# Optimization experiments

Measured on AMD Instinct MI355X. Metric: run time of the kernel, lower is better.

Reference implementation:

```python
import jax, jax.numpy as jnp
import numpy as np

NUM_SAMPLES = 128  # from __init__ default


def _trilinear_sample(vox, g):
    """grid_sample 5D, mode=bilinear (trilinear), padding_mode=zeros, align_corners=True.
    vox: [C, Dv, Hv, Wv]; g: [P, 3] normalized (x,y,z) with x->Wv, y->Hv, z->Dv.
    Returns [P, C]."""
    C, D, Hh, Ww = vox.shape
    x = (g[:, 0] + 1.0) * 0.5 * (Ww - 1)
    y = (g[:, 1] + 1.0) * 0.5 * (Hh - 1)
    z = (g[:, 2] + 1.0) * 0.5 * (D - 1)
    x0 = jnp.floor(x); y0 = jnp.floor(y); z0 = jnp.floor(z)
    xd = x - x0; yd = y - y0; zd = z - z0
    x0i = x0.astype(jnp.int32); y0i = y0.astype(jnp.int32); z0i = z0.astype(jnp.int32)
    out = jnp.zeros((g.shape[0], C), vox.dtype)
    for dz, wz in ((0, 1.0 - zd), (1, zd)):
        for dy, wy in ((0, 1.0 - yd), (1, yd)):
            for dx, wx in ((0, 1.0 - xd), (1, xd)):
                zi = z0i + dz; yi = y0i + dy; xi = x0i + dx
                valid = ((zi >= 0) & (zi < D) & (yi >= 0) & (yi < Hh) & (xi >= 0) & (xi < Ww)).astype(vox.dtype)
                zc = jnp.clip(zi, 0, D - 1); yc = jnp.clip(yi, 0, Hh - 1); xc = jnp.clip(xi, 0, Ww - 1)
                vals = vox[:, zc, yc, xc]  # [C, P]
                out = out + ((wz * wy * wx * valid)[:, None]) * vals.T
    return out


def setup_inputs() -> dict:
    key = jax.random.key(0)
    k1, k2 = jax.random.split(key)
    B, Hv, Wv, Dv = 4, 128, 128, 128
    H, W = 128, 128
    rgbsigma = jax.random.uniform(k1, (B, Hv, Wv, Dv, 4), dtype=jnp.float32)
    # cameras at ~z=3 looking down -z (identity rotation), slightly jittered
    pose = jnp.tile(jnp.eye(4, dtype=jnp.float32), (B, 1, 1))
    trans = jnp.array([0.0, 0.0, 3.0], dtype=jnp.float32) + 0.1 * jax.random.normal(k2, (B, 3), dtype=jnp.float32)
    pose = pose.at[:, :3, 3].set(trans)
    K = jnp.tile(jnp.array([[150.0, 0.0, 64.0], [0.0, 150.0, 64.0], [0.0, 0.0, 1.0]], dtype=jnp.float32), (B, 1, 1))
    bbox_min = jnp.tile(jnp.array([-1.0, -1.0, -1.0], dtype=jnp.float32), (B, 1))
    bbox_max = jnp.tile(jnp.array([1.0, 1.0, 1.0], dtype=jnp.float32), (B, 1))
    return {"rgbsigma": rgbsigma, "camera_pose": pose, "camera_intrinsics": K,
            "bbox_min": bbox_min, "bbox_max": bbox_max, "H": H, "W": W}


def reference(rgbsigma, camera_pose, camera_intrinsics, bbox_min, bbox_max, H, W):
    B = camera_pose.shape[0]
    N = H * W
    # --- ray generation ---
    ii, jj = jnp.meshgrid(jnp.arange(H, dtype=jnp.float32), jnp.arange(W, dtype=jnp.float32), indexing='ij')
    ii = ii.reshape(-1); jj = jj.reshape(-1)  # [N]
    fx = camera_intrinsics[:, 0, 0][:, None]; fy = camera_intrinsics[:, 1, 1][:, None]
    cx = camera_intrinsics[:, 0, 2][:, None]; cy = camera_intrinsics[:, 1, 2][:, None]
    dirs = jnp.stack([(jj[None, :] - cx) / fx, -(ii[None, :] - cy) / fy,
                      -jnp.ones((B, N), dtype=jnp.float32)], axis=-1)  # [B,N,3]
    rays_d = jnp.einsum('bij,bnj->bni', camera_pose[:, :3, :3], dirs)
    rays_d = rays_d / jnp.maximum(jnp.linalg.norm(rays_d, axis=-1, keepdims=True), 1e-12)
    rays_o = jnp.broadcast_to(camera_pose[:, None, :3, 3], (B, N, 3))
    # --- near/far via slab test ---
    inv_d = 1.0 / (rays_d + 1e-10)
    bmin = bbox_min[:, None, :]; bmax = bbox_max[:, None, :]
    t_min = (bmin - rays_o) * inv_d; t_max = (bmax - rays_o) * inv_d
    t1 = jnp.minimum(t_min, t_max); t2 = jnp.maximum(t_min, t_max)
    near = jnp.maximum(jnp.max(t1, axis=-1, keepdims=True), 0.1)
    far = jnp.maximum(jnp.min(t2, axis=-1, keepdims=True), near + 0.1)
    # --- stratified-uniform sample points ---
    t_vals = jnp.linspace(0.0, 1.0, NUM_SAMPLES, dtype=jnp.float32)
    z_vals = near + (far - near) * t_vals  # [B,N,M]
    pts = rays_o[:, :, None, :] + rays_d[:, :, None, :] * z_vals[..., None]  # [B,N,M,3]
    # --- trilinear voxel query ---
    scale = (bbox_max - bbox_min + 1e-10)[:, None, None, :]
    pts_norm = 2.0 * (pts - bbox_min[:, None, None, :]) / scale - 1.0
    vox = jnp.transpose(rgbsigma, (0, 4, 3, 1, 2))  # [B,4,Dv,Hv,Wv]
    sampled = jax.vmap(_trilinear_sample)(vox, pts_norm.reshape(B, N * NUM_SAMPLES, 3))
    sampled = sampled.reshape(B, N, NUM_SAMPLES, 4)
    rgb = sampled[..., :3]; sigma = sampled[..., 3]
    # --- alpha compositing ---
    dists = z_vals[..., 1:] - z_vals[..., :-1]
    dists = jnp.concatenate([dists, jnp.full_like(dists[..., :1], 1e10)], axis=-1)
    alpha = 1.0 - jnp.exp(-jax.nn.relu(sigma) * dists)
    trans = jnp.cumprod(jnp.concatenate([jnp.ones_like(alpha[..., :1]), 1.0 - alpha + 1e-10], axis=-1), axis=-1)[..., :-1]
    weights = alpha * trans
    rgb_map = jnp.sum(weights[..., None] * rgb, axis=-2)  # [B,N,3]
    acc_map = jnp.sum(weights, axis=-1)
    rgb_map = rgb_map + (1.0 - acc_map[..., None])  # white background
    return jnp.transpose(rgb_map.reshape(B, H, W, 3), (0, 3, 1, 2))
```

## Files before the change

### kernel.cpp

```cpp
#include <hip/hip_runtime.h>

#define NSAMP 128
#define VD 128
#define WPB 4

struct Corner8 {
    float4 v0, v1, v2, v3, v4, v5, v6, v7;
    float  w0, w1, w2, w3, w4, w5, w6, w7;
};

__device__ __forceinline__ void compute_ray_setup(
    int ray, int N, int W,
    const float* __restrict__ pose, const float* __restrict__ Kmat,
    const float* __restrict__ bmin, const float* __restrict__ bmax,
    float& axv, float& bxv, float& ayv, float& byv, float& azv, float& bzv,
    float& near, float& dt)
{
    const int b = ray / N;
    const int pix = ray - b * N;
    const int i = pix / W;
    const int j = pix - i * W;

    const float* P  = pose + b * 16;
    const float* Kb = Kmat + b * 9;
    const float fx = Kb[0], cx = Kb[2], fy = Kb[4], cy = Kb[5];

    const float dcx = ((float)j - cx) / fx;
    const float dcy = -((float)i - cy) / fy;
    const float dcz = -1.0f;

    float dx = P[0]*dcx + P[1]*dcy + P[2]*dcz;
    float dy = P[4]*dcx + P[5]*dcy + P[6]*dcz;
    float dz = P[8]*dcx + P[9]*dcy + P[10]*dcz;
    float nrm = sqrtf(dx*dx + dy*dy + dz*dz);
    nrm = fmaxf(nrm, 1e-12f);
    dx /= nrm; dy /= nrm; dz /= nrm;

    const float ox = P[3], oy = P[7], oz = P[11];

    const float bx0 = bmin[b*3+0], by0 = bmin[b*3+1], bz0 = bmin[b*3+2];
    const float bx1 = bmax[b*3+0], by1 = bmax[b*3+1], bz1 = bmax[b*3+2];

    const float ivx = 1.0f / (dx + 1e-10f);
    const float ivy = 1.0f / (dy + 1e-10f);
    const float ivz = 1.0f / (dz + 1e-10f);

    float ta, tb;
    ta = (bx0 - ox) * ivx; tb = (bx1 - ox) * ivx;
    const float t1x = fminf(ta, tb), t2x = fmaxf(ta, tb);
    ta = (by0 - oy) * ivy; tb = (by1 - oy) * ivy;
    const float t1y = fminf(ta, tb), t2y = fmaxf(ta, tb);
    ta = (bz0 - oz) * ivz; tb = (bz1 - oz) * ivz;
    const float t1z = fminf(ta, tb), t2z = fmaxf(ta, tb);

    near = fmaxf(fmaxf(t1x, fmaxf(t1y, t1z)), 0.1f);
    const float far = fmaxf(fminf(t2x, fminf(t2y, t2z)), near + 0.1f);

    const float sxs = (bx1 - bx0) + 1e-10f;
    const float sys = (by1 - by0) + 1e-10f;
    const float szs = (bz1 - bz0) + 1e-10f;
    const float C = (float)(VD - 1);
    axv = (ox - bx0) / sxs * C; bxv = dx / sxs * C;
    ayv = (oy - by0) / sys * C; byv = dy / sys * C;
    azv = (oz - bz0) / szs * C; bzv = dz / szs * C;

    dt = (far - near) * (1.0f / (float)(NSAMP - 1));
}

__global__ __launch_bounds__(256)
void RaySetup_kernel(const float* __restrict__ pose,
                     const float* __restrict__ Kmat,
                     const float* __restrict__ bmin,
                     const float* __restrict__ bmax,
                     const int* __restrict__ dH,
                     const int* __restrict__ dW,
                     float* __restrict__ rp,
                     int rays)
{
    const int ray = blockIdx.x * blockDim.x + threadIdx.x;
    if (ray >= rays) return;
    const int H = dH[0], W = dW[0];
    const int N = H * W;
    float axv, bxv, ayv, byv, azv, bzv, near, dt;
    compute_ray_setup(ray, N, W, pose, Kmat, bmin, bmax,
                      axv, bxv, ayv, byv, azv, bzv, near, dt);
    float4* o = reinterpret_cast<float4*>(rp + (size_t)ray * 8);
    o[0] = make_float4(axv, bxv, ayv, byv);
    o[1] = make_float4(azv, bzv, near, dt);
}

__device__ __forceinline__ void fetch_sample(
    Corner8& Bf, const float4* __restrict__ V4, float t,
    float axv, float bxv, float ayv, float byv, float azv, float bzv)
{
    const float xf = axv + bxv * t;
    const float yf = ayv + byv * t;
    const float zf = azv + bzv * t;
    const float x0f = floorf(xf), y0f = floorf(yf), z0f = floorf(zf);
    const float xd = xf - x0f, yd = yf - y0f, zd = zf - z0f;
    const int x0 = (int)x0f, y0 = (int)y0f, z0 = (int)z0f;
    const int x1 = x0 + 1, y1 = y0 + 1, z1 = z0 + 1;

    const int xc0 = min(max(x0, 0), VD - 1), xc1 = min(max(x1, 0), VD - 1);
    const int yc0 = min(max(y0, 0), VD - 1), yc1 = min(max(y1, 0), VD - 1);
    const int zc0 = min(max(z0, 0), VD - 1), zc1 = min(max(z1, 0), VD - 1);

    const float vx0 = (x0 == xc0) ? 1.0f : 0.0f;
    const float vx1 = (x1 == xc1) ? 1.0f : 0.0f;
    const float vy0 = (y0 == yc0) ? 1.0f : 0.0f;
    const float vy1 = (y1 == yc1) ? 1.0f : 0.0f;
    const float vz0 = (z0 == zc0) ? 1.0f : 0.0f;
    const float vz1 = (z1 == zc1) ? 1.0f : 0.0f;

    const float wx0 = (1.0f - xd) * vx0, wx1 = xd * vx1;
    const float wy0 = (1.0f - yd) * vy0, wy1 = yd * vy1;
    const float wz0 = (1.0f - zd) * vz0, wz1 = zd * vz1;

    const int r0 = yc0 << 14, r1 = yc1 << 14;
    const int c0 = xc0 << 7,  c1 = xc1 << 7;
    const int i00 = r0 + c0, i01 = r0 + c1;
    const int i10 = r1 + c0, i11 = r1 + c1;

    Bf.v0 = V4[i00 + zc0];
    Bf.v1 = V4[i00 + zc1];
    Bf.v2 = V4[i01 + zc0];
    Bf.v3 = V4[i01 + zc1];
    Bf.v4 = V4[i10 + zc0];
    Bf.v5 = V4[i10 + zc1];
    Bf.v6 = V4[i11 + zc0];
    Bf.v7 = V4[i11 + zc1];

    Bf.w0 = wy0 * wx0 * wz0;
    Bf.w1 = wy0 * wx0 * wz1;
    Bf.w2 = wy0 * wx1 * wz0;
    Bf.w3 = wy0 * wx1 * wz1;
    Bf.w4 = wy1 * wx0 * wz0;
    Bf.w5 = wy1 * wx0 * wz1;
    Bf.w6 = wy1 * wx1 * wz0;
    Bf.w7 = wy1 * wx1 * wz1;
}

__device__ __forceinline__ float4 interp_sample(const Corner8& Bf)
{
    float4 r;
    r.x = (Bf.w0*Bf.v0.x + Bf.w1*Bf.v1.x) + (Bf.w2*Bf.v2.x + Bf.w3*Bf.v3.x)
        + (Bf.w4*Bf.v4.x + Bf.w5*Bf.v5.x) + (Bf.w6*Bf.v6.x + Bf.w7*Bf.v7.x);
    r.y = (Bf.w0*Bf.v0.y + Bf.w1*Bf.v1.y) + (Bf.w2*Bf.v2.y + Bf.w3*Bf.v3.y)
        + (Bf.w4*Bf.v4.y + Bf.w5*Bf.v5.y) + (Bf.w6*Bf.v6.y + Bf.w7*Bf.v7.y);
    r.z = (Bf.w0*Bf.v0.z + Bf.w1*Bf.v1.z) + (Bf.w2*Bf.v2.z + Bf.w3*Bf.v3.z)
        + (Bf.w4*Bf.v4.z + Bf.w5*Bf.v5.z) + (Bf.w6*Bf.v6.z + Bf.w7*Bf.v7.z);
    r.w = (Bf.w0*Bf.v0.w + Bf.w1*Bf.v1.w) + (Bf.w2*Bf.v2.w + Bf.w3*Bf.v3.w)
        + (Bf.w4*Bf.v4.w + Bf.w5*Bf.v5.w) + (Bf.w6*Bf.v6.w + Bf.w7*Bf.v7.w);
    return r;
}

__device__ __forceinline__ float scan_prod64(float v, int lane)
{
    #pragma unroll
    for (int d = 1; d < 64; d <<= 1) {
        const float o = __shfl_up(v, d, 64);
        if (lane >= d) v *= o;
    }
    return v;
}

template <bool USE_WS>
__global__ __launch_bounds__(256, 1)
void VoxelRenderer_kernel(const float* __restrict__ vol,
                          const float* __restrict__ pose,
                          const float* __restrict__ Kmat,
                          const float* __restrict__ bmin,
                          const float* __restrict__ bmax,
                          const int* __restrict__ dH,
                          const int* __restrict__ dW,
                          const float* __restrict__ rayp,
                          float* __restrict__ out,
                          int rays)
{
    const int lane = threadIdx.x & 63;
    const int wid  = threadIdx.x >> 6;

    const int nwg = gridDim.x;
    const int bid = blockIdx.x;
    const int q = nwg >> 3, r = nwg & 7;
    const int xcd = bid & 7, idx = bid >> 3;
    const int swz = (xcd < r ? xcd * (q + 1) : r * (q + 1) + (xcd - r) * q) + idx;

    const int ray = swz * WPB + wid;
    if (ray >= rays) return;

    const int H = dH[0], W = dW[0];
    const int N = H * W;
    const int b = ray / N;
    const int pix = ray - b * N;

    float axv, bxv, ayv, byv, azv, bzv, near, dt;
    if (USE_WS) {
        const float4* p = reinterpret_cast<const float4*>(rayp + (size_t)ray * 8);
        const float4 p0 = p[0];
        const float4 p1 = p[1];
        axv = p0.x; bxv = p0.y; ayv = p0.z; byv = p0.w;
        azv = p1.x; bzv = p1.y; near = p1.z; dt = p1.w;
    } else {
        compute_ray_setup(ray, N, W, pose, Kmat, bmin, bmax,
                          axv, bxv, ayv, byv, azv, bzv, near, dt);
    }

    const float4* __restrict__ V4 =
        reinterpret_cast<const float4*>(vol + (size_t)b * VD * VD * VD * 4);

    const float tA = near + dt * (float)lane;
    const float tB = tA + dt * 64.0f;

    Corner8 A, Bf;
    fetch_sample(A,  V4, tA, axv, bxv, ayv, byv, azv, bzv);
    fetch_sample(Bf, V4, tB, axv, bxv, ayv, byv, azv, bzv);

    const float4 sA = interp_sample(A);
    const float sigA = fmaxf(sA.w, 0.0f);
    const float alphaA = 1.0f - __expf(-sigA * dt);
    const float tmA = 1.0f - alphaA + 1e-10f;

    float inclA = scan_prod64(tmA, lane);
    float PA = __shfl_up(inclA, 1, 64);
    if (lane == 0) PA = 1.0f;
    const float TtotA = __shfl(inclA, 63, 64);

    const float4 sB = interp_sample(Bf);
    const float sigB = fmaxf(sB.w, 0.0f);
    const float distB = (lane == 63) ? 1e10f : dt;
    const float alphaB = 1.0f - __expf(-sigB * distB);
    const float tmB = 1.0f - alphaB + 1e-10f;

    float inclB = scan_prod64(tmB, lane);
    float PB = __shfl_up(inclB, 1, 64);
    if (lane == 0) PB = 1.0f;
    const float TtotB = __shfl(inclB, 63, 64);

    const float wA = alphaA * PA;
    const float wB = alphaB * PB * TtotA;

    float R  = wA * sA.x + wB * sB.x;
    float G  = wA * sA.y + wB * sB.y;
    float Bl = wA * sA.z + wB * sB.z;

    #pragma unroll
    for (int d = 1; d < 64; d <<= 1) {
        R  += __shfl_xor(R,  d, 64);
        G  += __shfl_xor(G,  d, 64);
        Bl += __shfl_xor(Bl, d, 64);
    }

    if (lane == 0) {
        const float bg = TtotA * TtotB;
        float* outb = out + (size_t)b * 3 * N + pix;
        outb[0 * (size_t)N] = R + bg;
        outb[1 * (size_t)N] = G + bg;
        outb[2 * (size_t)N] = Bl + bg;
    }
}

extern "C" void kernel_launch(void* const* d_in, const int* in_sizes, int n_in,
                              void* d_out, int out_size, void* d_ws, size_t ws_size,
                              hipStream_t stream) {
    const float* rgbsigma = (const float*)d_in[0];
    const float* pose     = (const float*)d_in[1];
    const float* Kmat     = (const float*)d_in[2];
    const float* bmin     = (const float*)d_in[3];
    const float* bmax     = (const float*)d_in[4];
    const int*   dH       = (const int*)d_in[5];
    const int*   dW       = (const int*)d_in[6];
    float* out = (float*)d_out;

    const int rays = out_size / 3;
    const int grid = (rays + WPB - 1) / WPB;
    const bool use_ws = ws_size >= (size_t)rays * 8 * sizeof(float);

    if (use_ws) {
        float* rp = (float*)d_ws;
        RaySetup_kernel<<<(rays + 255) / 256, 256, 0, stream>>>(
            pose, Kmat, bmin, bmax, dH, dW, rp, rays);
        VoxelRenderer_kernel<true><<<grid, 64 * WPB, 0, stream>>>(
            rgbsigma, pose, Kmat, bmin, bmax, dH, dW, rp, out, rays);
    } else {
        VoxelRenderer_kernel<false><<<grid, 64 * WPB, 0, stream>>>(
            rgbsigma, pose, Kmat, bmin, bmax, dH, dW, nullptr, out, rays);
    }
}
```

Before: 62.91 us.

## Render 2x2 pixel quads per wavefront with 16-lane segmented sample scans

Each 64-lane wavefront now handles a 2x2 quad of neighbouring pixels, 16 lanes per ray, instead of one ray per wavefront. Each ray walks its 128 samples in 8 chunks of 16, double-buffering the corner fetches and carrying transmittance across chunks with a 16-wide product scan. The aim is better cache locality from neighbouring rays touching nearby voxels, and shorter scans and reductions. In exchange each lane does serial work across chunks and holds more registers for the two Corner8 buffers. It also assumes W and the ray count are even.

New measurement: 56.40 us, median of 2. 1.12x faster.

```diff
diff --git a/kernel.cpp b/kernel.cpp
--- a/kernel.cpp
+++ b/kernel.cpp
@@ -2,7 +2,6 @@
 
 #define NSAMP 128
 #define VD 128
-#define WPB 4
 
 struct Corner8 {
     float4 v0, v1, v2, v3, v4, v5, v6, v7;
@@ -154,14 +153,31 @@
     return r;
 }
 
-__device__ __forceinline__ float scan_prod64(float v, int lane)
-{
+__device__ __forceinline__ void consume_set(
+    const Corner8& C, int k, float dt, int sl,
+    float& Tcarry, float& accR, float& accG, float& accB)
+{
+    const float4 s = interp_sample(C);
+    const float sig = fmaxf(s.w, 0.0f);
+    const float dist = (k == NSAMP - 1) ? 1e10f : dt;
+    const float alpha = 1.0f - __expf(-sig * dist);
+    float incl = 1.0f - alpha + 1e-10f;
+
     #pragma unroll
-    for (int d = 1; d < 64; d <<= 1) {
-        const float o = __shfl_up(v, d, 64);
-        if (lane >= d) v *= o;
-    }
-    return v;
+    for (int d = 1; d < 16; d <<= 1) {
+        const float o = __shfl_up(incl, d, 16);
+        if (sl >= d) incl *= o;
+    }
+    float P = __shfl_up(incl, 1, 16);
+    if (sl == 0) P = 1.0f;
+
+    const float w = alpha * P * Tcarry;
+    accR += w * s.x;
+    accG += w * s.y;
+    accB += w * s.z;
+
+    const float Ttot = __shfl(incl, 15, 16);
+    Tcarry *= Ttot;
 }
 
 template <bool USE_WS>
@@ -178,7 +194,9 @@
                           int rays)
 {
     const int lane = threadIdx.x & 63;
-    const int wid  = threadIdx.x >> 6;
+    const int wq   = threadIdx.x >> 6;
+    const int rq   = lane >> 4;
+    const int sl   = lane & 15;
 
     const int nwg = gridDim.x;
     const int bid = blockIdx.x;
@@ -186,13 +204,21 @@
     const int xcd = bid & 7, idx = bid >> 3;
     const int swz = (xcd < r ? xcd * (q + 1) : r * (q + 1) + (xcd - r) * q) + idx;
 
-    const int ray = swz * WPB + wid;
-    if (ray >= rays) return;
-
     const int H = dH[0], W = dW[0];
     const int N = H * W;
-    const int b = ray / N;
-    const int pix = ray - b * N;
+    const int quads = rays >> 2;
+    const int qid = swz * 4 + wq;
+    if (qid >= quads) return;
+
+    const int qPerImg = N >> 2;
+    const int b   = qid / qPerImg;
+    const int rem = qid - b * qPerImg;
+    const int halfW = W >> 1;
+    const int qi = rem / halfW;
+    const int qj = rem - qi * halfW;
+    const int i = qi * 2 + (rq >> 1);
+    const int j = qj * 2 + (rq & 1);
+    const int ray = b * N + i * W + j;
 
     float axv, bxv, ayv, byv, azv, bzv, near, dt;
     if (USE_WS) {
@@ -209,54 +235,36 @@
     const float4* __restrict__ V4 =
         reinterpret_cast<const float4*>(vol + (size_t)b * VD * VD * VD * 4);
 
-    const float tA = near + dt * (float)lane;
-    const float tB = tA + dt * 64.0f;
+    float Tcarry = 1.0f;
+    float accR = 0.0f, accG = 0.0f, accB = 0.0f;
 
     Corner8 A, Bf;
-    fetch_sample(A,  V4, tA, axv, bxv, ayv, byv, azv, bzv);
-    fetch_sample(Bf, V4, tB, axv, bxv, ayv, byv, azv, bzv);
-
-    const float4 sA = interp_sample(A);
-    const float sigA = fmaxf(sA.w, 0.0f);
-    const float alphaA = 1.0f - __expf(-sigA * dt);
-    const float tmA = 1.0f - alphaA + 1e-10f;
-
-    float inclA = scan_prod64(tmA, lane);
-    float PA = __shfl_up(inclA, 1, 64);
-    if (lane == 0) PA = 1.0f;
-    const float TtotA = __shfl(inclA, 63, 64);
-
-    const float4 sB = interp_sample(Bf);
-    const float sigB = fmaxf(sB.w, 0.0f);
-    const float distB = (lane == 63) ? 1e10f : dt;
-    const float alphaB = 1.0f - __expf(-sigB * distB);
-    const float tmB = 1.0f - alphaB + 1e-10f;
-
-    float inclB = scan_prod64(tmB, lane);
-    float PB = __shfl_up(inclB, 1, 64);
-    if (lane == 0) PB = 1.0f;
-    const float TtotB = __shfl(inclB, 63, 64);
-
-    const float wA = alphaA * PA;
-    const float wB = alphaB * PB * TtotA;
-
-    float R  = wA * sA.x + wB * sB.x;
-    float G  = wA * sA.y + wB * sB.y;
-    float Bl = wA * sA.z + wB * sB.z;
+    fetch_sample(A, V4, near + dt * (float)sl, axv, bxv, ayv, byv, azv, bzv);
 
     #pragma unroll
-    for (int d = 1; d < 64; d <<= 1) {
-        R  += __shfl_xor(R,  d, 64);
-        G  += __shfl_xor(G,  d, 64);
-        Bl += __shfl_xor(Bl, d, 64);
-    }
-
-    if (lane == 0) {
-        const float bg = TtotA * TtotB;
-        float* outb = out + (size_t)b * 3 * N + pix;
-        outb[0 * (size_t)N] = R + bg;
-        outb[1 * (size_t)N] = G + bg;
-        outb[2 * (size_t)N] = Bl + bg;
+    for (int st = 0; st < 8; st += 2) {
+        fetch_sample(Bf, V4, near + dt * (float)((st + 1) * 16 + sl),
+                     axv, bxv, ayv, byv, azv, bzv);
+        consume_set(A, st * 16 + sl, dt, sl, Tcarry, accR, accG, accB);
+        if (st + 2 < 8)
+            fetch_sample(A, V4, near + dt * (float)((st + 2) * 16 + sl),
+                         axv, bxv, ayv, byv, azv, bzv);
+        consume_set(Bf, (st + 1) * 16 + sl, dt, sl, Tcarry, accR, accG, accB);
+    }
+
+    #pragma unroll
+    for (int d = 1; d < 16; d <<= 1) {
+        accR += __shfl_xor(accR, d, 16);
+        accG += __shfl_xor(accG, d, 16);
+        accB += __shfl_xor(accB, d, 16);
+    }
+
+    if (sl == 0) {
+        const float bg = Tcarry;
+        float* outb = out + (size_t)b * 3 * N + i * W + j;
+        outb[0 * (size_t)N] = accR + bg;
+        outb[1 * (size_t)N] = accG + bg;
+        outb[2 * (size_t)N] = accB + bg;
     }
 }
 
@@ -272,18 +280,19 @@
     const int*   dW       = (const int*)d_in[6];
     float* out = (float*)d_out;
 
-    const int rays = out_size / 3;
-    const int grid = (rays + WPB - 1) / WPB;
+    const int rays  = out_size / 3;
+    const int quads = rays / 4;
+    const int grid  = (quads + 3) / 4;
     const bool use_ws = ws_size >= (size_t)rays * 8 * sizeof(float);
 
     if (use_ws) {
         float* rp = (float*)d_ws;
         RaySetup_kernel<<<(rays + 255) / 256, 256, 0, stream>>>(
             pose, Kmat, bmin, bmax, dH, dW, rp, rays);
-        VoxelRenderer_kernel<true><<<grid, 64 * WPB, 0, stream>>>(
+        VoxelRenderer_kernel<true><<<grid, 256, 0, stream>>>(
             rgbsigma, pose, Kmat, bmin, bmax, dH, dW, rp, out, rays);
     } else {
-        VoxelRenderer_kernel<false><<<grid, 64 * WPB, 0, stream>>>(
+        VoxelRenderer_kernel<false><<<grid, 256, 0, stream>>>(
             rgbsigma, pose, Kmat, bmin, bmax, dH, dW, nullptr, out, rays);
     }
 }
```
